# Optimization experiments

Measured on AMD Instinct MI355X. Metric: run time of the kernel, lower is better.

## Reference

```python
import jax, jax.numpy as jnp
import numpy as np

P = 8  # patch_size hard-coded in the module


def conv1x1(x, W, b):
    # x: [B,C,H,W_], W: [O,C], b: [O]  (1x1 conv == per-pixel linear)
    return jnp.einsum('oc,bchw->bohw', W, x) + b[None, :, None, None]


def to_patch_tokens(t):
    # Replicates t.unfold(2,P,P).unfold(3,P,P).contiguous().view(B,-1,N)
    # t: [B,Cq,W,H] -> [B, Cq*P*P, N] with N = (W//P)*(H//P)
    B, Cq, Wd, Hd = t.shape
    Wp, Hp = Wd // P, Hd // P
    t = t.reshape(B, Cq, Wp, P, Hp, P).transpose(0, 1, 2, 4, 3, 5)  # [B,Cq,Wp,Hp,P,P]
    return t.reshape(B, Cq * P * P, Wp * Hp)


def setup_inputs() -> dict:
    key = jax.random.key(0)
    ks = jax.random.split(key, 10)
    B, C, Wd, Hd = 8, 64, 256, 256
    Cq = C // 8
    s_in = 1.0 / np.sqrt(C)
    s_out = 1.0 / np.sqrt(Cq)
    return {
        'x': jax.random.normal(ks[0], (B, C, Wd, Hd), jnp.float32),
        'Wq': jax.random.normal(ks[1], (Cq, C), jnp.float32) * s_in,
        'bq': jax.random.normal(ks[2], (Cq,), jnp.float32) * 0.01,
        'Wk': jax.random.normal(ks[3], (Cq, C), jnp.float32) * s_in,
        'bk': jax.random.normal(ks[4], (Cq,), jnp.float32) * 0.01,
        'Wv': jax.random.normal(ks[5], (Cq, C), jnp.float32) * s_in,
        'bv': jax.random.normal(ks[6], (Cq,), jnp.float32) * 0.01,
        'Wo': jax.random.normal(ks[7], (C, Cq), jnp.float32) * s_out,
        'bo': jax.random.normal(ks[8], (C,), jnp.float32) * 0.01,
        'gamma': jax.random.normal(ks[9], (1,), jnp.float32),
    }


def reference(x, Wq, bq, Wk, bk, Wv, bv, Wo, bo, gamma):
    B, C, Wd, Hd = x.shape
    Cq = C // 8
    q = to_patch_tokens(conv1x1(x, Wq, bq)).transpose(0, 2, 1)  # [B,N,M]
    k = to_patch_tokens(conv1x1(x, Wk, bk))                     # [B,M,N]
    v = to_patch_tokens(conv1x1(x, Wv, bv))                     # [B,M,N]
    N = k.shape[-1]  # d_k in source == number of patch tokens
    energy = jnp.einsum('bnm,bmk->bnk', q, k) / jnp.sqrt(jnp.float32(N))
    attn = jax.nn.softmax(energy, axis=-1)                      # [B,N,N]
    out = jnp.einsum('bmn,bjn->bmj', v, attn)                   # bmm(v, attn^T)
    out = out.transpose(0, 2, 1).reshape(B, Cq, Wd, Hd)
    out = conv1x1(out, Wo, bo)
    return gamma * out + x
```

## Files before the change

### kernel.cpp

```cpp
#include <hip/hip_runtime.h>
#include <stdint.h>

typedef unsigned short u16;
typedef unsigned int   u32;
typedef __attribute__((ext_vector_type(8))) short  short8;
typedef __attribute__((ext_vector_type(4))) float  floatx4;

__device__ __forceinline__ u16 f32_to_bf16(float f) {
  u32 u = __builtin_bit_cast(u32, f);
  u = (u + 0x7fffu + ((u >> 16) & 1u)) >> 16;
  return (u16)u;
}
__device__ __forceinline__ float bf16_to_f32(u16 h) {
  u32 u = ((u32)h) << 16;
  return __builtin_bit_cast(float, u);
}
__device__ __forceinline__ u32 pack2(float a, float b) {
  return (u32)f32_to_bf16(a) | ((u32)f32_to_bf16(b) << 16);
}

__device__ __forceinline__ void load_lds16(const u16* g, u16* l) {
  auto gp = (const __attribute__((address_space(1))) u32*)(uintptr_t)g;
  auto lp = (__attribute__((address_space(3))) u32*)(u32)(uintptr_t)l;
  __builtin_amdgcn_global_load_lds(gp, lp, 16, 0, 0);
}

__global__ __launch_bounds__(256) void qkv_kernel(
    const float* __restrict__ x,
    const float* __restrict__ Wq, const float* __restrict__ bq,
    const float* __restrict__ Wk, const float* __restrict__ bk,
    const float* __restrict__ Wv, const float* __restrict__ bv,
    u16* __restrict__ qt, u16* __restrict__ kt, u16* __restrict__ vm)
{
  __shared__ __align__(16) u16 qs[128 * 64];
  __shared__ __align__(16) u16 ks_[128 * 64];
  __shared__ __align__(16) u16 vs[64 * 128];

  const int wq = blockIdx.x;
  const int g  = blockIdx.y;
  const int b  = blockIdx.z;
  const int t  = threadIdx.x;
  const int wl = t >> 3;
  const int hg = t & 7;
  const int strip = hg >> 2, hq = hg & 3;
  const int w  = wq * 32 + wl;
  const int h0 = g * 16 + strip * 128 + hq * 4;

  float aq[4][8], ak[4][8], av[4][8];
#pragma unroll
  for (int j = 0; j < 4; j++)
#pragma unroll
    for (int i = 0; i < 8; i++) { aq[j][i] = 0.f; ak[j][i] = 0.f; av[j][i] = 0.f; }

  const float* xp = x + (size_t)b * 64 * 65536 + w * 256 + h0;
#pragma unroll 4
  for (int c = 0; c < 64; c++) {
    const float4 xv = *(const float4*)(xp + (size_t)c * 65536);
    const float xs[4] = {xv.x, xv.y, xv.z, xv.w};
#pragma unroll
    for (int cq = 0; cq < 8; cq++) {
      const float wqv = Wq[cq * 64 + c];
      const float wkv = Wk[cq * 64 + c];
      const float wvv = Wv[cq * 64 + c];
#pragma unroll
      for (int j = 0; j < 4; j++) {
        aq[j][cq] = fmaf(wqv, xs[j], aq[j][cq]);
        ak[j][cq] = fmaf(wkv, xs[j], ak[j][cq]);
        av[j][cq] = fmaf(wvv, xs[j], av[j][cq]);
      }
    }
  }

  const int mc = (wl >> 3) * 2 + strip;
#pragma unroll
  for (int j = 0; j < 4; j++) {
    const int h  = h0 + j;
    const int nl = ((h >> 3) & 1) * 64 + (w & 7) * 8 + (h & 7);
#pragma unroll
    for (int cq = 0; cq < 8; cq++) {
      qs[nl * 64 + cq * 8 + mc]    = f32_to_bf16(aq[j][cq] + bq[cq]);
      ks_[nl * 64 + cq * 8 + mc]   = f32_to_bf16(ak[j][cq] + bk[cq]);
      vs[(cq * 8 + mc) * 128 + nl] = f32_to_bf16(av[j][cq] + bv[cq]);
    }
  }
  __syncthreads();

#pragma unroll
  for (int i = 0; i < 4; i++) {
    const int idx = i * 256 + t;
    const int nl2 = idx >> 3, cq2 = idx & 7;
    const size_t row = (size_t)b * 1024 + g * 128 + nl2;
    *(uint4*)(qt + row * 512 + cq2 * 64 + wq * 8) = *(const uint4*)(qs + nl2 * 64 + cq2 * 8);
    *(uint4*)(kt + row * 512 + cq2 * 64 + wq * 8) = *(const uint4*)(ks_ + nl2 * 64 + cq2 * 8);
    const int pr = idx >> 4, l16 = idx & 15;
    const int mrow = (pr >> 3) * 64 + wq * 8 + (pr & 7);
    *(uint4*)(vm + ((size_t)b * 512 + mrow) * 1024 + g * 128 + l16 * 8) =
        *(const uint4*)(vs + pr * 128 + l16 * 8);
  }
}

template <int FMW>
__global__ __launch_bounds__(256) void gemm_nt(
    const u16* __restrict__ A, const u16* __restrict__ Bm, u16* __restrict__ Cm,
    int M, int N, int K, float scale)
{
  constexpr int BM = FMW * 32;
  __shared__ __align__(16) u16 As[2][BM * 64];
  __shared__ __align__(16) u16 Bs[2][128 * 64];

  const int bz = blockIdx.x, bn = blockIdx.y, bm = blockIdx.z;
  const int t = threadIdx.x;
  const int lane = t & 63, wid = t >> 6;
  const int wm = wid & 1, wn = wid >> 1;
  const int m0 = bm * BM, n0 = bn * 128;

  const u16* Ab = A + (size_t)bz * M * K + (size_t)m0 * K;
  const u16* Bb = Bm + (size_t)bz * N * K + (size_t)n0 * K;

  floatx4 acc[FMW][4];
#pragma unroll
  for (int i = 0; i < FMW; i++)
#pragma unroll
    for (int j = 0; j < 4; j++) acc[i][j] = (floatx4){0.f, 0.f, 0.f, 0.f};

  const int srow = wid * 8 + (lane >> 3);
  const int scol = (((lane & 7) ^ ((lane >> 3) & 7)) << 3);
  const int l15 = lane & 15, quad = lane >> 4;
  const int cxor = (l15 & 7) << 3;

#pragma unroll
  for (int i = 0; i < FMW; i++)
    load_lds16(Ab + (size_t)(i * 32 + srow) * K + scol, As[0] + (i * 32 + wid * 8) * 64);
#pragma unroll
  for (int i = 0; i < 4; i++)
    load_lds16(Bb + (size_t)(i * 32 + srow) * K + scol, Bs[0] + (i * 32 + wid * 8) * 64);
  __syncthreads();

  const int nk = K >> 6;
#pragma unroll 2
  for (int kk = 0; kk < nk; kk++) {
    const int cur = kk & 1;
    if (kk + 1 < nk) {
      const int k1 = (kk + 1) << 6;
#pragma unroll
      for (int i = 0; i < FMW; i++)
        load_lds16(Ab + (size_t)(i * 32 + srow) * K + k1 + scol,
                   As[cur ^ 1] + (i * 32 + wid * 8) * 64);
#pragma unroll
      for (int i = 0; i < 4; i++)
        load_lds16(Bb + (size_t)(i * 32 + srow) * K + k1 + scol,
                   Bs[cur ^ 1] + (i * 32 + wid * 8) * 64);
    }
#pragma unroll
    for (int ks = 0; ks < 2; ks++) {
      const int koff = (ks * 32 + quad * 8) ^ cxor;
      short8 a[FMW], b[4];
#pragma unroll
      for (int f = 0; f < FMW; f++)
        a[f] = *(const short8*)(As[cur] + (wm * FMW * 16 + f * 16 + l15) * 64 + koff);
#pragma unroll
      for (int f = 0; f < 4; f++)
        b[f] = *(const short8*)(Bs[cur] + (wn * 64 + f * 16 + l15) * 64 + koff);
#pragma unroll
      for (int fm = 0; fm < FMW; fm++)
#pragma unroll
        for (int fn = 0; fn < 4; fn++)
          acc[fm][fn] = __builtin_amdgcn_mfma_f32_16x16x32_bf16(a[fm], b[fn], acc[fm][fn], 0, 0, 0);
    }
    __syncthreads();
  }

  u16* Cb = Cm + (size_t)bz * M * N;
#pragma unroll
  for (int fm = 0; fm < FMW; fm++)
#pragma unroll
    for (int fn = 0; fn < 4; fn++)
#pragma unroll
      for (int r = 0; r < 4; r++) {
        int row = m0 + wm * FMW * 16 + fm * 16 + quad * 4 + r;
        int col = n0 + wn * 64 + fn * 16 + l15;
        Cb[(size_t)row * N + col] = f32_to_bf16(scale * acc[fm][fn][r]);
      }
}

__global__ __launch_bounds__(256) void softmax_kernel(u16* __restrict__ EP)
{
  const int r = (blockIdx.x << 2) + (threadIdx.x >> 6);
  const int lane = threadIdx.x & 63;
  u16* row = EP + (size_t)r * 1024;
  const uint4* rp = (const uint4*)row;

  uint4 v0 = rp[lane * 2];
  uint4 v1 = rp[lane * 2 + 1];
  const u32 wds[8] = {v0.x, v0.y, v0.z, v0.w, v1.x, v1.y, v1.z, v1.w};
  float e[16];
#pragma unroll
  for (int i = 0; i < 8; i++) {
    e[2 * i]     = bf16_to_f32((u16)wds[i]);
    e[2 * i + 1] = bf16_to_f32((u16)(wds[i] >> 16));
  }

  float mx = e[0];
#pragma unroll
  for (int i = 1; i < 16; i++) mx = fmaxf(mx, e[i]);
#pragma unroll
  for (int off = 32; off > 0; off >>= 1) mx = fmaxf(mx, __shfl_xor(mx, off));

  float s = 0.f;
#pragma unroll
  for (int i = 0; i < 16; i++) { e[i] = __expf(e[i] - mx); s += e[i]; }
#pragma unroll
  for (int off = 32; off > 0; off >>= 1) s += __shfl_xor(s, off);

  const float inv = 1.0f / s;
  uint4 o0, o1;
  o0.x = pack2(e[0] * inv,  e[1] * inv);
  o0.y = pack2(e[2] * inv,  e[3] * inv);
  o0.z = pack2(e[4] * inv,  e[5] * inv);
  o0.w = pack2(e[6] * inv,  e[7] * inv);
  o1.x = pack2(e[8] * inv,  e[9] * inv);
  o1.y = pack2(e[10] * inv, e[11] * inv);
  o1.z = pack2(e[12] * inv, e[13] * inv);
  o1.w = pack2(e[14] * inv, e[15] * inv);
  ((uint4*)row)[lane * 2]     = o0;
  ((uint4*)row)[lane * 2 + 1] = o1;
}

__global__ __launch_bounds__(256) void out_kernel(
    const float* __restrict__ x, const u16* __restrict__ OT,
    const float* __restrict__ Wo, const float* __restrict__ bo,
    const float* __restrict__ gammap, float* __restrict__ out)
{
  const int q4 = blockIdx.x * 256 + threadIdx.x;
  const int b = q4 >> 14;
  const int rem = (q4 & 16383) * 4;
  const float gmv = gammap[0];

  const u16* otb = OT + (size_t)b * 524288;
  const int m0 = rem & 511;
  const int nbase = rem >> 9;
  float oc[8][4];
#pragma unroll
  for (int cq = 0; cq < 8; cq++) {
    ushort4 hv = *(const ushort4*)(otb + (size_t)(cq * 128 + nbase) * 512 + m0);
    oc[cq][0] = bf16_to_f32(hv.x);
    oc[cq][1] = bf16_to_f32(hv.y);
    oc[cq][2] = bf16_to_f32(hv.z);
    oc[cq][3] = bf16_to_f32(hv.w);
  }

  const float* xb = x + (size_t)b * 4194304 + rem;
  float* ob = out + (size_t)b * 4194304 + rem;
#pragma unroll 4
  for (int o = 0; o < 64; o++) {
    const float4 xv = *(const float4*)(xb + (size_t)o * 65536);
    const float bv = bo[o];
    float a0 = bv, a1 = bv, a2 = bv, a3 = bv;
#pragma unroll
    for (int cq = 0; cq < 8; cq++) {
      const float wv = Wo[o * 8 + cq];
      a0 = fmaf(wv, oc[cq][0], a0);
      a1 = fmaf(wv, oc[cq][1], a1);
      a2 = fmaf(wv, oc[cq][2], a2);
      a3 = fmaf(wv, oc[cq][3], a3);
    }
    float4 rv;
    rv.x = fmaf(gmv, a0, xv.x);
    rv.y = fmaf(gmv, a1, xv.y);
    rv.z = fmaf(gmv, a2, xv.z);
    rv.w = fmaf(gmv, a3, xv.w);
    *(float4*)(ob + (size_t)o * 65536) = rv;
  }
}

extern "C" void kernel_launch(void* const* d_in, const int* in_sizes, int n_in,
                              void* d_out, int out_size, void* d_ws, size_t ws_size,
                              hipStream_t stream) {
  const float* x  = (const float*)d_in[0];
  const float* Wq = (const float*)d_in[1];
  const float* bq = (const float*)d_in[2];
  const float* Wk = (const float*)d_in[3];
  const float* bk = (const float*)d_in[4];
  const float* Wv = (const float*)d_in[5];
  const float* bv = (const float*)d_in[6];
  const float* Wo = (const float*)d_in[7];
  const float* bo = (const float*)d_in[8];
  const float* gm = (const float*)d_in[9];
  float* out = (float*)d_out;

  u16* qt = (u16*)d_ws;
  u16* kt = qt + 4194304;
  u16* vm = kt + 4194304;
  u16* EP = vm + 4194304;
  u16* OT = qt;

  qkv_kernel<<<dim3(8, 8, 8), 256, 0, stream>>>(x, Wq, bq, Wk, bk, Wv, bv, qt, kt, vm);
  gemm_nt<4><<<dim3(8, 8, 8), 256, 0, stream>>>(qt, kt, EP, 1024, 1024, 512, 0.03125f);
  softmax_kernel<<<2048, 256, 0, stream>>>(EP);
  gemm_nt<2><<<dim3(8, 4, 16), 256, 0, stream>>>(EP, vm, OT, 1024, 512, 1024, 1.0f);
  out_kernel<<<512, 256, 0, stream>>>(x, OT, Wo, bo, gm, out);
}
```

Baseline: 346.7 us.

## Double threads per block in QKV and GEMM kernels; split output-projection channels

The QKV projection now uses 512 threads, each computing two pixels instead of four. It caches the biases in registers and writes q/k to padded LDS with vectorized 16-byte stores, then gathers them back with strided reads. Both GEMMs run 8 waves per block, each wave owning a 32-column slice instead of 64, which halves accumulator registers per wave. The output kernel launches 4x more blocks, each handling two pixels and half of the output channels. The aim is more latency hiding through higher parallelism, at the cost of less register-level reuse and more LDS reads per MFMA.

```diff
diff --git a/kernel.cpp b/kernel.cpp
--- a/kernel.cpp
+++ b/kernel.cpp
@@ -25,73 +25,95 @@
   __builtin_amdgcn_global_load_lds(gp, lp, 16, 0, 0);
 }
 
-__global__ __launch_bounds__(256) void qkv_kernel(
+__global__ __launch_bounds__(512) void qkv_kernel(
     const float* __restrict__ x,
     const float* __restrict__ Wq, const float* __restrict__ bq,
     const float* __restrict__ Wk, const float* __restrict__ bk,
     const float* __restrict__ Wv, const float* __restrict__ bv,
     u16* __restrict__ qt, u16* __restrict__ kt, u16* __restrict__ vm)
 {
-  __shared__ __align__(16) u16 qs[128 * 64];
-  __shared__ __align__(16) u16 ks_[128 * 64];
+  __shared__ __align__(16) u16 qs[128 * 72];
+  __shared__ __align__(16) u16 ks_[128 * 72];
   __shared__ __align__(16) u16 vs[64 * 128];
 
   const int wq = blockIdx.x;
   const int g  = blockIdx.y;
   const int b  = blockIdx.z;
   const int t  = threadIdx.x;
-  const int wl = t >> 3;
-  const int hg = t & 7;
-  const int strip = hg >> 2, hq = hg & 3;
+  const int wl = t >> 4;
+  const int hg = t & 15;
+  const int strip = hg >> 3, hq = hg & 7;
   const int w  = wq * 32 + wl;
-  const int h0 = g * 16 + strip * 128 + hq * 4;
-
-  float aq[4][8], ak[4][8], av[4][8];
-#pragma unroll
-  for (int j = 0; j < 4; j++)
+  const int h0 = g * 16 + strip * 128 + hq * 2;
+
+  float bqr[8], bkr[8], bvr[8];
+#pragma unroll
+  for (int i = 0; i < 8; i++) { bqr[i] = bq[i]; bkr[i] = bk[i]; bvr[i] = bv[i]; }
+
+  float aq[2][8], ak[2][8], av[2][8];
+#pragma unroll
+  for (int j = 0; j < 2; j++)
 #pragma unroll
     for (int i = 0; i < 8; i++) { aq[j][i] = 0.f; ak[j][i] = 0.f; av[j][i] = 0.f; }
 
   const float* xp = x + (size_t)b * 64 * 65536 + w * 256 + h0;
 #pragma unroll 4
   for (int c = 0; c < 64; c++) {
-    const float4 xv = *(const float4*)(xp + (size_t)c * 65536);
-    const float xs[4] = {xv.x, xv.y, xv.z, xv.w};
+    const float2 xv = *(const float2*)(xp + (size_t)c * 65536);
 #pragma unroll
     for (int cq = 0; cq < 8; cq++) {
       const float wqv = Wq[cq * 64 + c];
       const float wkv = Wk[cq * 64 + c];
       const float wvv = Wv[cq * 64 + c];
-#pragma unroll
-      for (int j = 0; j < 4; j++) {
-        aq[j][cq] = fmaf(wqv, xs[j], aq[j][cq]);
-        ak[j][cq] = fmaf(wkv, xs[j], ak[j][cq]);
-        av[j][cq] = fmaf(wvv, xs[j], av[j][cq]);
-      }
+      aq[0][cq] = fmaf(wqv, xv.x, aq[0][cq]);
+      aq[1][cq] = fmaf(wqv, xv.y, aq[1][cq]);
+      ak[0][cq] = fmaf(wkv, xv.x, ak[0][cq]);
+      ak[1][cq] = fmaf(wkv, xv.y, ak[1][cq]);
+      av[0][cq] = fmaf(wvv, xv.x, av[0][cq]);
+      av[1][cq] = fmaf(wvv, xv.y, av[1][cq]);
     }
   }
 
-  const int mc = (wl >> 3) * 2 + strip;
-#pragma unroll
-  for (int j = 0; j < 4; j++) {
+  const int mc = ((wl >> 3) & 3) * 2 + strip;
+#pragma unroll
+  for (int j = 0; j < 2; j++) {
     const int h  = h0 + j;
     const int nl = ((h >> 3) & 1) * 64 + (w & 7) * 8 + (h & 7);
-#pragma unroll
-    for (int cq = 0; cq < 8; cq++) {
-      qs[nl * 64 + cq * 8 + mc]    = f32_to_bf16(aq[j][cq] + bq[cq]);
-      ks_[nl * 64 + cq * 8 + mc]   = f32_to_bf16(ak[j][cq] + bk[cq]);
-      vs[(cq * 8 + mc) * 128 + nl] = f32_to_bf16(av[j][cq] + bv[cq]);
-    }
+    uint4 qv, kv;
+    qv.x = pack2(aq[j][0] + bqr[0], aq[j][1] + bqr[1]);
+    qv.y = pack2(aq[j][2] + bqr[2], aq[j][3] + bqr[3]);
+    qv.z = pack2(aq[j][4] + bqr[4], aq[j][5] + bqr[5]);
+    qv.w = pack2(aq[j][6] + bqr[6], aq[j][7] + bqr[7]);
+    kv.x = pack2(ak[j][0] + bkr[0], ak[j][1] + bkr[1]);
+    kv.y = pack2(ak[j][2] + bkr[2], ak[j][3] + bkr[3]);
+    kv.z = pack2(ak[j][4] + bkr[4], ak[j][5] + bkr[5]);
+    kv.w = pack2(ak[j][6] + bkr[6], ak[j][7] + bkr[7]);
+    *(uint4*)(qs  + nl * 72 + mc * 8) = qv;
+    *(uint4*)(ks_ + nl * 72 + mc * 8) = kv;
+#pragma unroll
+    for (int cq = 0; cq < 8; cq++)
+      vs[(cq * 8 + mc) * 128 + nl] = f32_to_bf16(av[j][cq] + bvr[cq]);
   }
   __syncthreads();
 
 #pragma unroll
-  for (int i = 0; i < 4; i++) {
-    const int idx = i * 256 + t;
+  for (int i = 0; i < 2; i++) {
+    const int idx = i * 512 + t;
     const int nl2 = idx >> 3, cq2 = idx & 7;
     const size_t row = (size_t)b * 1024 + g * 128 + nl2;
-    *(uint4*)(qt + row * 512 + cq2 * 64 + wq * 8) = *(const uint4*)(qs + nl2 * 64 + cq2 * 8);
-    *(uint4*)(kt + row * 512 + cq2 * 64 + wq * 8) = *(const uint4*)(ks_ + nl2 * 64 + cq2 * 8);
+    const u16* qr = qs  + nl2 * 72 + cq2;
+    const u16* kr = ks_ + nl2 * 72 + cq2;
+    uint4 qv, kv;
+    qv.x = (u32)qr[0]  | ((u32)qr[8]  << 16);
+    qv.y = (u32)qr[16] | ((u32)qr[24] << 16);
+    qv.z = (u32)qr[32] | ((u32)qr[40] << 16);
+    qv.w = (u32)qr[48] | ((u32)qr[56] << 16);
+    kv.x = (u32)kr[0]  | ((u32)kr[8]  << 16);
+    kv.y = (u32)kr[16] | ((u32)kr[24] << 16);
+    kv.z = (u32)kr[32] | ((u32)kr[40] << 16);
+    kv.w = (u32)kr[48] | ((u32)kr[56] << 16);
+    *(uint4*)(qt + row * 512 + cq2 * 64 + wq * 8) = qv;
+    *(uint4*)(kt + row * 512 + cq2 * 64 + wq * 8) = kv;
     const int pr = idx >> 4, l16 = idx & 15;
     const int mrow = (pr >> 3) * 64 + wq * 8 + (pr & 7);
     *(uint4*)(vm + ((size_t)b * 512 + mrow) * 1024 + g * 128 + l16 * 8) =
@@ -100,11 +122,12 @@
 }
 
 template <int FMW>
-__global__ __launch_bounds__(256) void gemm_nt(
+__global__ __launch_bounds__(512) void gemm_nt(
     const u16* __restrict__ A, const u16* __restrict__ Bm, u16* __restrict__ Cm,
     int M, int N, int K, float scale)
 {
   constexpr int BM = FMW * 32;
+  constexpr int NA = BM / 64;
   __shared__ __align__(16) u16 As[2][BM * 64];
   __shared__ __align__(16) u16 Bs[2][128 * 64];
 
@@ -117,11 +140,11 @@
   const u16* Ab = A + (size_t)bz * M * K + (size_t)m0 * K;
   const u16* Bb = Bm + (size_t)bz * N * K + (size_t)n0 * K;
 
-  floatx4 acc[FMW][4];
+  floatx4 acc[FMW][2];
 #pragma unroll
   for (int i = 0; i < FMW; i++)
 #pragma unroll
-    for (int j = 0; j < 4; j++) acc[i][j] = (floatx4){0.f, 0.f, 0.f, 0.f};
+    for (int j = 0; j < 2; j++) acc[i][j] = (floatx4){0.f, 0.f, 0.f, 0.f};
 
   const int srow = wid * 8 + (lane >> 3);
   const int scol = (((lane & 7) ^ ((lane >> 3) & 7)) << 3);
@@ -129,11 +152,11 @@
   const int cxor = (l15 & 7) << 3;
 
 #pragma unroll
-  for (int i = 0; i < FMW; i++)
-    load_lds16(Ab + (size_t)(i * 32 + srow) * K + scol, As[0] + (i * 32 + wid * 8) * 64);
-#pragma unroll
-  for (int i = 0; i < 4; i++)
-    load_lds16(Bb + (size_t)(i * 32 + srow) * K + scol, Bs[0] + (i * 32 + wid * 8) * 64);
+  for (int i = 0; i < NA; i++)
+    load_lds16(Ab + (size_t)(i * 64 + srow) * K + scol, As[0] + (i * 64 + wid * 8) * 64);
+#pragma unroll
+  for (int i = 0; i < 2; i++)
+    load_lds16(Bb + (size_t)(i * 64 + srow) * K + scol, Bs[0] + (i * 64 + wid * 8) * 64);
   __syncthreads();
 
   const int nk = K >> 6;
@@ -143,28 +166,28 @@
     if (kk + 1 < nk) {
       const int k1 = (kk + 1) << 6;
 #pragma unroll
-      for (int i = 0; i < FMW; i++)
-        load_lds16(Ab + (size_t)(i * 32 + srow) * K + k1 + scol,
-                   As[cur ^ 1] + (i * 32 + wid * 8) * 64);
-#pragma unroll
-      for (int i = 0; i < 4; i++)
-        load_lds16(Bb + (size_t)(i * 32 + srow) * K + k1 + scol,
-                   Bs[cur ^ 1] + (i * 32 + wid * 8) * 64);
+      for (int i = 0; i < NA; i++)
+        load_lds16(Ab + (size_t)(i * 64 + srow) * K + k1 + scol,
+                   As[cur ^ 1] + (i * 64 + wid * 8) * 64);
+#pragma unroll
+      for (int i = 0; i < 2; i++)
+        load_lds16(Bb + (size_t)(i * 64 + srow) * K + k1 + scol,
+                   Bs[cur ^ 1] + (i * 64 + wid * 8) * 64);
     }
 #pragma unroll
     for (int ks = 0; ks < 2; ks++) {
       const int koff = (ks * 32 + quad * 8) ^ cxor;
-      short8 a[FMW], b[4];
+      short8 a[FMW], b[2];
 #pragma unroll
       for (int f = 0; f < FMW; f++)
         a[f] = *(const short8*)(As[cur] + (wm * FMW * 16 + f * 16 + l15) * 64 + koff);
 #pragma unroll
-      for (int f = 0; f < 4; f++)
-        b[f] = *(const short8*)(Bs[cur] + (wn * 64 + f * 16 + l15) * 64 + koff);
+      for (int f = 0; f < 2; f++)
+        b[f] = *(const short8*)(Bs[cur] + (wn * 32 + f * 16 + l15) * 64 + koff);
 #pragma unroll
       for (int fm = 0; fm < FMW; fm++)
 #pragma unroll
-        for (int fn = 0; fn < 4; fn++)
+        for (int fn = 0; fn < 2; fn++)
           acc[fm][fn] = __builtin_amdgcn_mfma_f32_16x16x32_bf16(a[fm], b[fn], acc[fm][fn], 0, 0, 0);
     }
     __syncthreads();
@@ -174,11 +197,11 @@
 #pragma unroll
   for (int fm = 0; fm < FMW; fm++)
 #pragma unroll
-    for (int fn = 0; fn < 4; fn++)
+    for (int fn = 0; fn < 2; fn++)
 #pragma unroll
       for (int r = 0; r < 4; r++) {
         int row = m0 + wm * FMW * 16 + fm * 16 + quad * 4 + r;
-        int col = n0 + wn * 64 + fn * 16 + l15;
+        int col = n0 + wn * 32 + fn * 16 + l15;
         Cb[(size_t)row * N + col] = f32_to_bf16(scale * acc[fm][fn][r]);
       }
 }
@@ -231,45 +254,44 @@
     const float* __restrict__ Wo, const float* __restrict__ bo,
     const float* __restrict__ gammap, float* __restrict__ out)
 {
-  const int q4 = blockIdx.x * 256 + threadIdx.x;
-  const int b = q4 >> 14;
-  const int rem = (q4 & 16383) * 4;
+  const int gb = blockIdx.x;
+  const int osel = gb & 1;
+  const int q2 = (gb >> 1) * 256 + threadIdx.x;
+  const int b = q2 >> 15;
+  const int rem = (q2 & 32767) * 2;
   const float gmv = gammap[0];
 
   const u16* otb = OT + (size_t)b * 524288;
   const int m0 = rem & 511;
   const int nbase = rem >> 9;
-  float oc[8][4];
+  float oc[8][2];
 #pragma unroll
   for (int cq = 0; cq < 8; cq++) {
-    ushort4 hv = *(const ushort4*)(otb + (size_t)(cq * 128 + nbase) * 512 + m0);
+    ushort2 hv = *(const ushort2*)(otb + (size_t)(cq * 128 + nbase) * 512 + m0);
     oc[cq][0] = bf16_to_f32(hv.x);
     oc[cq][1] = bf16_to_f32(hv.y);
-    oc[cq][2] = bf16_to_f32(hv.z);
-    oc[cq][3] = bf16_to_f32(hv.w);
-  }
-
-  const float* xb = x + (size_t)b * 4194304 + rem;
-  float* ob = out + (size_t)b * 4194304 + rem;
+  }
+
+  const size_t obase = (size_t)b * 4194304 + rem + (size_t)osel * 32 * 65536;
+  const float* xb = x + obase;
+  float* ob = out + obase;
+  const int o0 = osel * 32;
 #pragma unroll 4
-  for (int o = 0; o < 64; o++) {
-    const float4 xv = *(const float4*)(xb + (size_t)o * 65536);
+  for (int oo = 0; oo < 32; oo++) {
+    const int o = o0 + oo;
+    const float2 xv = *(const float2*)(xb + (size_t)oo * 65536);
     const float bv = bo[o];
-    float a0 = bv, a1 = bv, a2 = bv, a3 = bv;
+    float a0 = bv, a1 = bv;
 #pragma unroll
     for (int cq = 0; cq < 8; cq++) {
       const float wv = Wo[o * 8 + cq];
       a0 = fmaf(wv, oc[cq][0], a0);
       a1 = fmaf(wv, oc[cq][1], a1);
-      a2 = fmaf(wv, oc[cq][2], a2);
-      a3 = fmaf(wv, oc[cq][3], a3);
     }
-    float4 rv;
+    float2 rv;
     rv.x = fmaf(gmv, a0, xv.x);
     rv.y = fmaf(gmv, a1, xv.y);
-    rv.z = fmaf(gmv, a2, xv.z);
-    rv.w = fmaf(gmv, a3, xv.w);
-    *(float4*)(ob + (size_t)o * 65536) = rv;
+    *(float2*)(ob + (size_t)oo * 65536) = rv;
   }
 }
 
@@ -294,9 +316,9 @@
   u16* EP = vm + 4194304;
   u16* OT = qt;
 
-  qkv_kernel<<<dim3(8, 8, 8), 256, 0, stream>>>(x, Wq, bq, Wk, bk, Wv, bv, qt, kt, vm);
-  gemm_nt<4><<<dim3(8, 8, 8), 256, 0, stream>>>(qt, kt, EP, 1024, 1024, 512, 0.03125f);
+  qkv_kernel<<<dim3(8, 8, 8), 512, 0, stream>>>(x, Wq, bq, Wk, bk, Wv, bv, qt, kt, vm);
+  gemm_nt<4><<<dim3(8, 8, 8), 512, 0, stream>>>(qt, kt, EP, 1024, 1024, 512, 0.03125f);
   softmax_kernel<<<2048, 256, 0, stream>>>(EP);
-  gemm_nt<2><<<dim3(8, 4, 16), 256, 0, stream>>>(EP, vm, OT, 1024, 512, 1024, 1.0f);
-  out_kernel<<<512, 256, 0, stream>>>(x, OT, Wo, bo, gm, out);
-}
+  gemm_nt<2><<<dim3(8, 4, 16), 512, 0, stream>>>(EP, vm, OT, 1024, 512, 1024, 1.0f);
+  out_kernel<<<2048, 256, 0, stream>>>(x, OT, Wo, bo, gm, out);
+}
```

New measurement: 334.3 us. 1.04x faster.
